# Kernel optimization log

Measured on AMD Instinct MI355X. Metric: run time of the kernel, lower is better.

The kernel has to match this reference:

```python
import jax, jax.numpy as jnp
import numpy as np
from functools import partial

D_MODEL = 1024
D_STATE = 16
D_CONV = 4
EXPAND = 2
DIM = EXPAND * D_MODEL  # 2048


def setup_inputs() -> dict:
    key = jax.random.key(0)
    ks = jax.random.split(key, 10)
    s = lambda fan_in: 1.0 / np.sqrt(fan_in)
    inp = {
        "x": jax.random.normal(ks[0], (8, 2048, D_MODEL), dtype=jnp.float32),
        "W_in": jax.random.normal(ks[1], (DIM, D_MODEL), dtype=jnp.float32) * s(D_MODEL),
        "b_in": jnp.zeros((DIM,), dtype=jnp.float32),
        "conv_w": jax.random.normal(ks[2], (DIM, 1, D_CONV), dtype=jnp.float32) * s(D_CONV),
        "conv_b": jnp.zeros((DIM,), dtype=jnp.float32),
        "W_x": jax.random.normal(ks[3], (3 * D_STATE, DIM), dtype=jnp.float32) * s(DIM),
        "W_dt": jax.random.normal(ks[4], (DIM, D_STATE), dtype=jnp.float32) * s(D_STATE),
        "b_dt": jnp.zeros((DIM,), dtype=jnp.float32),
        "W_out": jax.random.normal(ks[5], (D_MODEL, DIM), dtype=jnp.float32) * s(DIM),
        "b_out": jnp.zeros((D_MODEL,), dtype=jnp.float32),
    }
    return inp


def _selective_scan(xc, delta, A, Bm, Cm):
    # xc, delta: (B, L, DIM); Bm, Cm: (B, L, N); A: (N,)
    Bsz = xc.shape[0]
    h0 = jnp.zeros((Bsz, DIM, D_STATE), dtype=xc.dtype)

    def step(h, inputs):
        xc_t, d_t, b_t, c_t = inputs  # (B,DIM),(B,DIM),(B,N),(B,N)
        h = h * jnp.exp(d_t[:, :, None] * A) + xc_t[:, :, None] * b_t[:, None, :]
        y_t = jnp.einsum("bdn,bn->bd", h, c_t)
        return h, y_t

    tm = lambda a: jnp.swapaxes(a, 0, 1)  # time-major
    _, ys = jax.lax.scan(step, h0, (tm(xc), tm(delta), tm(Bm), tm(Cm)))
    return jnp.swapaxes(ys, 0, 1)  # (B, L, DIM)


def reference(x, W_in, b_in, conv_w, conv_b, W_x, W_dt, b_dt, W_out, b_out):
    A = -jnp.exp(jnp.linspace(0.0, -5.0, D_STATE).astype(x.dtype))  # (N,)
    xp = x @ W_in.T + b_in  # (B, L, DIM)
    # depthwise conv1d, padding=D_CONV-1 on BOTH sides (as torch Conv1d) -> length L+D_CONV-1
    xc = jax.lax.conv_general_dilated(
        jnp.swapaxes(xp, 1, 2), conv_w,
        window_strides=(1,), padding=[(D_CONV - 1, D_CONV - 1)],
        feature_group_count=DIM,
        dimension_numbers=("NCH", "OIH", "NCH"),
    ) + conv_b[None, :, None]
    xc = jnp.swapaxes(xc, 1, 2)  # (B, Lc, DIM)
    x_dbl = xc @ W_x.T  # (B, Lc, 3N)
    d_raw, Bm, Cm = jnp.split(x_dbl, [D_STATE, 2 * D_STATE], axis=-1)
    delta = jax.nn.softplus(d_raw @ W_dt.T + b_dt)  # (B, Lc, DIM)
    y = _selective_scan(xc, delta, A, Bm, Cm)  # (B, Lc, DIM)
    return y @ W_out.T + b_out  # (B, Lc, D_MODEL)
```

## Files before the change

### kernel.cpp

```cpp
#include <hip/hip_runtime.h>
#include <cstdint>
#include <cstddef>

#define B8 8
#define LSEQ 2048
#define LC 2051
#define DMODEL 1024
#define DIM 2048
#define LPAD 2054
#define M2 16408
#define M2P 16512
#define CS 32
#define NCH 65

typedef __attribute__((ext_vector_type(8))) short short8;
typedef __attribute__((ext_vector_type(4))) float floatx4;
typedef __attribute__((ext_vector_type(2))) float float2v;
typedef __attribute__((address_space(3))) unsigned short lds_ushort;

__device__ __constant__ float AeT[16] = {
  -1.0f,          -0.71653131f, -0.51341712f, -0.36787944f,
  -0.26359714f,   -0.18887560f, -0.13533528f, -0.09697208f,
  -0.06948345f,   -0.04978707f, -0.03567399f, -0.02556154f,
  -0.01831564f,   -0.01312373f, -0.00940356f, -0.00673795f};

#define LOG2E 1.44269504088896f

__device__ __forceinline__ float bf2f(unsigned short h) {
  union { unsigned int u; float f; } v; v.u = ((unsigned int)h) << 16; return v.f;
}
__device__ __forceinline__ unsigned short f2bf(float f) {
  union { float f; unsigned int u; } v; v.f = f;
  unsigned int r = (v.u + 0x7FFFu + ((v.u >> 16) & 1u)) >> 16;
  return (unsigned short)r;
}

__device__ __forceinline__ float2v pk_mul_vv(float2v a, float2v b) {
  float2v d; asm("v_pk_mul_f32 %0, %1, %2" : "=v"(d) : "v"(a), "v"(b)); return d;
}
__device__ __forceinline__ float2v pk_mul_sv(float2v bs, float2v a) {
  float2v d; asm("v_pk_mul_f32 %0, %1, %2" : "=v"(d) : "s"(bs), "v"(a)); return d;
}
__device__ __forceinline__ float2v pk_fma_vvv(float2v a, float2v b, float2v c) {
  float2v d; asm("v_pk_fma_f32 %0, %1, %2, %3" : "=v"(d) : "v"(a), "v"(b), "v"(c)); return d;
}
__device__ __forceinline__ float2v pk_fma_vsv(float2v a, float2v bs, float2v c) {
  float2v d; asm("v_pk_fma_f32 %0, %1, %2, %3" : "=v"(d) : "v"(a), "s"(bs), "v"(c)); return d;
}
__device__ __forceinline__ float2v pk_add_vv(float2v a, float2v b) {
  float2v d; asm("v_pk_add_f32 %0, %1, %2" : "=v"(d) : "v"(a), "v"(b)); return d;
}
__device__ __forceinline__ float exp2_raw(float x) {
  float d; asm("v_exp_f32 %0, %1" : "=v"(d) : "v"(x)); return d;
}

__device__ __forceinline__ short8 ds_read_b128_(const lds_ushort* p) {
  floatx4 d;
  unsigned addr = (unsigned)(size_t)p;
  asm volatile("ds_read_b128 %0, %1" : "=v"(d) : "v"(addr));
  return __builtin_bit_cast(short8, d);
}

__global__ __launch_bounds__(256) void init_kernel(const float* __restrict__ x,
                                                   const float* __restrict__ W_in,
                                                   const float* __restrict__ W_out,
                                                   const float* __restrict__ W_x,
                                                   unsigned short* __restrict__ xA,
                                                   unsigned short* __restrict__ wInB,
                                                   unsigned short* __restrict__ wOutB,
                                                   unsigned short* __restrict__ wXB,
                                                   unsigned short* __restrict__ xp) {
  const int gid = blockIdx.x;
  const float* in; unsigned short* out; int i;
  if (gid < 8192)        { in = x;     out = xA;    i = gid * 256 + threadIdx.x; }
  else if (gid < 9216)   { in = W_in;  out = wInB;  i = (gid - 8192) * 256 + threadIdx.x; }
  else if (gid < 10240)  { in = W_out; out = wOutB; i = (gid - 9216) * 256 + threadIdx.x; }
  else if (gid < 10288)  { in = W_x;   out = wXB;   i = (gid - 10240) * 256 + threadIdx.x; }
  else {
    int ii = (gid - 10288) * 256 + threadIdx.x;
    int b = ii / 1536;
    int r6 = (ii % 1536) / 256;
    int dd = (ii % 256) * 8;
    int row = (r6 < 3) ? r6 : (2048 + r6);
    *(uint4*)(xp + ((size_t)b * LPAD + row) * DIM + dd) = make_uint4(0, 0, 0, 0);
    return;
  }
  const float4* p = (const float4*)in + (size_t)i * 2;
  float4 a = p[0], b = p[1];
  uint4 o;
  o.x = (unsigned)f2bf(a.x) | ((unsigned)f2bf(a.y) << 16);
  o.y = (unsigned)f2bf(a.z) | ((unsigned)f2bf(a.w) << 16);
  o.z = (unsigned)f2bf(b.x) | ((unsigned)f2bf(b.y) << 16);
  o.w = (unsigned)f2bf(b.z) | ((unsigned)f2bf(b.w) << 16);
  *((uint4*)out + i) = o;
}

__global__ __launch_bounds__(256) void conv_kernel(const unsigned short* __restrict__ xp,
                                                   const float* __restrict__ conv_w,
                                                   const float* __restrict__ conv_b,
                                                   unsigned short* __restrict__ xc) {
  const int tc0 = blockIdx.x * 16;
  const int b = blockIdx.y;
  const int d0 = threadIdx.x * 8;

  float4 cw[8];
#pragma unroll
  for (int j = 0; j < 8; ++j) cw[j] = *(const float4*)(conv_w + (size_t)(d0 + j) * 4);
  float cb[8];
  {
    const float4* cb4 = (const float4*)(conv_b + d0);
    float4 c0 = cb4[0], c1 = cb4[1];
    cb[0] = c0.x; cb[1] = c0.y; cb[2] = c0.z; cb[3] = c0.w;
    cb[4] = c1.x; cb[5] = c1.y; cb[6] = c1.z; cb[7] = c1.w;
  }

  const unsigned short* base = xp + ((size_t)b * LPAD + tc0) * DIM + d0;
  unsigned short* outp = xc + ((size_t)b * LC + tc0) * DIM + d0;

  auto loadrow = [&](float (&w)[8], int r) {
    uint4 v = *(const uint4*)(base + (size_t)r * DIM);
    w[0] = bf2f(v.x & 0xffff); w[1] = bf2f(v.x >> 16);
    w[2] = bf2f(v.y & 0xffff); w[3] = bf2f(v.y >> 16);
    w[4] = bf2f(v.z & 0xffff); w[5] = bf2f(v.z >> 16);
    w[6] = bf2f(v.w & 0xffff); w[7] = bf2f(v.w >> 16);
  };

  float wa[8], wb[8], wc[8];
  loadrow(wa, 0); loadrow(wb, 1); loadrow(wc, 2);
#pragma unroll
  for (int i = 0; i < 16; ++i) {
    float wd[8];
    loadrow(wd, i + 3);
    if (tc0 + i < LC) {
      float acc[8];
#pragma unroll
      for (int j = 0; j < 8; ++j) {
        acc[j] = cb[j];
        acc[j] = fmaf(wa[j], cw[j].x, acc[j]);
        acc[j] = fmaf(wb[j], cw[j].y, acc[j]);
        acc[j] = fmaf(wc[j], cw[j].z, acc[j]);
        acc[j] = fmaf(wd[j], cw[j].w, acc[j]);
      }
      uint4 o;
      o.x = (unsigned)f2bf(acc[0]) | ((unsigned)f2bf(acc[1]) << 16);
      o.y = (unsigned)f2bf(acc[2]) | ((unsigned)f2bf(acc[3]) << 16);
      o.z = (unsigned)f2bf(acc[4]) | ((unsigned)f2bf(acc[5]) << 16);
      o.w = (unsigned)f2bf(acc[6]) | ((unsigned)f2bf(acc[7]) << 16);
      *(uint4*)(outp + (size_t)i * DIM) = o;
    }
#pragma unroll
    for (int j = 0; j < 8; ++j) { wa[j] = wb[j]; wb[j] = wc[j]; wc[j] = wd[j]; }
  }
}

#define GAS(p) ((const __attribute__((address_space(1))) void*)(p))
#define LAS(p) ((__attribute__((address_space(3))) void*)(p))

template <int MODE, int NBM, int NBN, int LX, int TAIL, int SPLITK>
__global__ __launch_bounds__(256) void gemm_bt(const unsigned short* __restrict__ A,
                                               const unsigned short* __restrict__ Bw,
                                               const float* __restrict__ bias,
                                               void* __restrict__ Cout, int K) {
  const int gid = blockIdx.x;
  const int mainBlocks = 8 * LX * NBN;
  int bm, bn, ks = 0;
  if constexpr (SPLITK) {
    ks = gid & 7;
    bm = gid >> 3;
    bn = 0;
  } else if (TAIL && gid >= mainBlocks) {
    const int e = gid - mainBlocks;
    bm = 8 * LX + e / NBN;
    bn = e % NBN;
  } else {
    const int xcd = gid & 7;
    const int j = gid >> 3;
    bm = xcd * LX + (j % LX);
    bn = j / LX;
  }
  if (bm >= NBM) return;

  __shared__ __align__(16) unsigned short As[2][128 * 64];
  __shared__ __align__(16) unsigned short Bs[2][128 * 64];
  const int tid = threadIdx.x;
  const int lane = tid & 63, wave = tid >> 6;
  const int wr = wave >> 1, wc = wave & 1;

  floatx4 acc[4][4];
#pragma unroll
  for (int i = 0; i < 4; ++i)
#pragma unroll
    for (int j2 = 0; j2 < 4; ++j2) acc[i][j2] = (floatx4){0.f, 0.f, 0.f, 0.f};

  const int srow = tid >> 3;
  const int scol = ((tid & 7) ^ ((tid >> 3) & 7)) * 8;
  const unsigned short* Ab[4];
  const unsigned short* Bb[4];
#pragma unroll
  for (int L = 0; L < 4; ++L) {
    Ab[L] = A  + (size_t)(bm * 128 + L * 32 + srow) * K + scol;
    Bb[L] = Bw + (size_t)(bn * 128 + L * 32 + srow) * K + scol;
  }

  const int fr = lane & 15;
  const int hi = lane >> 4;
  const int fx = fr & 7;

  auto STAGE = [&](int buf, int k0) {
#pragma unroll
    for (int L = 0; L < 4; ++L) {
      __builtin_amdgcn_global_load_lds(GAS(Ab[L] + k0), LAS(&As[buf][L * 2048 + tid * 8]), 16, 0, 0);
      __builtin_amdgcn_global_load_lds(GAS(Bb[L] + k0), LAS(&Bs[buf][L * 2048 + tid * 8]), 16, 0, 0);
    }
  };

  const int kbase = SPLITK ? ks * (K >> 3) : 0;
  const int NT = (SPLITK ? (K >> 3) : K) >> 6;
  STAGE(0, kbase);
  asm volatile("s_waitcnt vmcnt(0)");
  __syncthreads();

  int cur = 0;
  for (int t = 0; t < NT; ++t) {
    if (t + 1 < NT) STAGE(cur ^ 1, kbase + (t + 1) * 64);

    const lds_ushort* tA = (const lds_ushort*)LAS(&As[cur][0]);
    const lds_ushort* tB = (const lds_ushort*)LAS(&Bs[cur][0]);
#pragma unroll
    for (int kk = 0; kk < 2; ++kk) {
      const int pb = ((kk * 4 + hi) ^ fx) * 8;
      short8 af[4], bf[4];
#pragma unroll
      for (int mt = 0; mt < 4; ++mt) af[mt] = ds_read_b128_(tA + (wr * 64 + mt * 16 + fr) * 64 + pb);
#pragma unroll
      for (int nt = 0; nt < 4; ++nt) bf[nt] = ds_read_b128_(tB + (wc * 64 + nt * 16 + fr) * 64 + pb);
      asm volatile("s_waitcnt lgkmcnt(0)");
      __builtin_amdgcn_sched_barrier(0);
      __builtin_amdgcn_s_setprio(1);
#pragma unroll
      for (int mt = 0; mt < 4; ++mt)
#pragma unroll
        for (int nt = 0; nt < 4; ++nt)
          acc[mt][nt] = __builtin_amdgcn_mfma_f32_16x16x32_bf16(af[mt], bf[nt], acc[mt][nt], 0, 0, 0);
      __builtin_amdgcn_s_setprio(0);
    }
    __syncthreads();
    cur ^= 1;
  }

  const int er = (lane >> 4) * 4, ec = lane & 15;
#pragma unroll
  for (int mt = 0; mt < 4; ++mt) {
#pragma unroll
    for (int nt = 0; nt < 4; ++nt) {
#pragma unroll
      for (int i = 0; i < 4; ++i) {
        int r = bm * 128 + wr * 64 + mt * 16 + er + i;
        int c = bn * 128 + wc * 64 + nt * 16 + ec;
        float v = acc[mt][nt][i];
        if constexpr (MODE == 0) {
          int bb = r >> 11, t = r & 2047;
          ((unsigned short*)Cout)[((size_t)bb * LPAD + 3 + t) * DIM + c] = f2bf(v + bias[c]);
        } else if constexpr (MODE == 1) {
          if (c < 48) ((float*)Cout)[((size_t)ks * M2P + r) * 48 + c] = v;
        } else {
          if (r < M2) ((float*)Cout)[(size_t)r * DMODEL + c] = v + bias[c];
        }
      }
    }
  }
}

__global__ __launch_bounds__(256) void reduce_xdbl(const float* __restrict__ part,
                                                   float* __restrict__ xdbl) {
  int i = blockIdx.x * 256 + threadIdx.x;
  if (i >= 196896) return;
  float4 s = make_float4(0.f, 0.f, 0.f, 0.f);
#pragma unroll
  for (int ks = 0; ks < 8; ++ks) {
    float4 v = *(const float4*)(part + (size_t)ks * M2P * 48 + (size_t)i * 4);
    s.x += v.x; s.y += v.y; s.z += v.z; s.w += v.w;
  }
  *(float4*)(xdbl + (size_t)i * 4) = s;
}

__global__ __launch_bounds__(256) void delta_kernel(const float* __restrict__ xdbl,
                                                    const float* __restrict__ W_dt,
                                                    const float* __restrict__ b_dt,
                                                    unsigned short* __restrict__ delta) {
  const int d = blockIdx.y * 256 + threadIdx.x;
  const int r0 = blockIdx.x * 8;
  float wv[16];
  const float4* wp = (const float4*)(W_dt + (size_t)d * 16);
#pragma unroll
  for (int q = 0; q < 4; ++q) {
    float4 t = wp[q];
    wv[q * 4 + 0] = t.x; wv[q * 4 + 1] = t.y; wv[q * 4 + 2] = t.z; wv[q * 4 + 3] = t.w;
  }
  const float bd = b_dt[d];
#pragma unroll
  for (int j = 0; j < 8; ++j) {
    const float* dr = xdbl + (size_t)(r0 + j) * 48;
    float z0 = bd, z1 = 0.f, z2 = 0.f, z3 = 0.f;
#pragma unroll
    for (int n = 0; n < 16; n += 4) {
      z0 = fmaf(dr[n + 0], wv[n + 0], z0);
      z1 = fmaf(dr[n + 1], wv[n + 1], z1);
      z2 = fmaf(dr[n + 2], wv[n + 2], z2);
      z3 = fmaf(dr[n + 3], wv[n + 3], z3);
    }
    float z = (z0 + z1) + (z2 + z3);
    float dl = (z > 20.f) ? z : __logf(1.f + __expf(z));
    delta[(size_t)(r0 + j) * DIM + d] = f2bf(dl);
  }
}

__global__ __launch_bounds__(256) void scan_pass1(const unsigned short* __restrict__ xc,
                                                  const unsigned short* __restrict__ dl,
                                                  const float* __restrict__ xd,
                                                  unsigned short* __restrict__ sdbuf,
                                                  unsigned short* __restrict__ qbuf) {
  const int wid = __builtin_amdgcn_readfirstlane((int)(threadIdx.x >> 6));
  const int lane = threadIdx.x & 63;
  const int W = blockIdx.x * 4 + wid;
  const int dg = W & 31;
  const int rest = W >> 5;
  const int c = rest % NCH;
  const int b = rest / NCH;
  const int d = dg * 64 + lane;
  const int t0 = c * CS;
  const int nst = (t0 + CS <= LC) ? CS : (LC - t0);

  float2v A2L[8];
#pragma unroll
  for (int i = 0; i < 8; ++i)
    A2L[i] = (float2v){AeT[2 * i] * LOG2E, AeT[2 * i + 1] * LOG2E};

  float2v h2[8];
#pragma unroll
  for (int i = 0; i < 8; ++i) h2[i] = (float2v){0.f, 0.f};
  float sumd = 0.f;

  const size_t row0 = (size_t)b * LC + t0;
  const float* xdb = xd + row0 * 48 + 16;
  const unsigned short* xcp = xc + row0 * DIM + d;
  const unsigned short* dp  = dl + row0 * DIM + d;

  auto body = [&](int s) {
    float2v Bv[8];
#pragma unroll
    for (int j = 0; j < 8; ++j) Bv[j] = *(const float2v*)(xdb + (size_t)s * 48 + 2 * j);
    float dlt = bf2f(dp[(size_t)s * DIM]);
    float xcv = bf2f(xcp[(size_t)s * DIM]);
    sumd += dlt;
    float2v dlt2 = (float2v){dlt, dlt};
    float2v xcv2 = (float2v){xcv, xcv};
#pragma unroll
    for (int i = 0; i < 8; ++i) {
      float2v arg = pk_mul_vv(dlt2, A2L[i]);
      float e0 = exp2_raw(arg.x), e1 = exp2_raw(arg.y);
      float2v e2 = (float2v){e0, e1};
      h2[i] = pk_fma_vvv(h2[i], e2, pk_mul_sv(Bv[i], xcv2));
    }
  };

  if (nst == CS) {
#pragma unroll
    for (int s = 0; s < CS; ++s) body(s);
  } else {
    for (int s = 0; s < nst; ++s) body(s);
  }

  sdbuf[((size_t)(b * NCH + c) << 11) + d] = f2bf(sumd);
  const size_t base = ((size_t)(b * NCH + c) * 16) * 2048 + d;
#pragma unroll
  for (int i = 0; i < 8; ++i) {
    qbuf[base + ((size_t)(2 * i) << 11)]     = f2bf(h2[i].x);
    qbuf[base + ((size_t)(2 * i + 1) << 11)] = f2bf(h2[i].y);
  }
}

__global__ __launch_bounds__(256) void scan_boundary(const unsigned short* __restrict__ sdbuf,
                                                     unsigned short* __restrict__ qbuf) {
  const int tid = threadIdx.x;
  const int n = tid >> 4;
  const int d = blockIdx.x * 16 + (tid & 15);
  const int b = blockIdx.y;
  const float aL = AeT[n] * LOG2E;
  float h = 0.f;
  for (int c = 0; c < NCH; ++c) {
    const size_t sbase = ((size_t)(b * NCH + c) << 11);
    const float sd = bf2f(sdbuf[sbase + d]);
    const size_t base = (sbase << 4) + ((size_t)n << 11) + d;
    const float qv = bf2f(qbuf[base]);
    const float Pv = exp2_raw(sd * aL);
    qbuf[base] = f2bf(h);
    h = fmaf(Pv, h, qv);
  }
}

__global__ __launch_bounds__(256) void scan_pass2(const unsigned short* __restrict__ xc,
                                                  const unsigned short* __restrict__ dl,
                                                  const float* __restrict__ xd,
                                                  const unsigned short* __restrict__ hinit,
                                                  unsigned short* __restrict__ y) {
  const int wid = __builtin_amdgcn_readfirstlane((int)(threadIdx.x >> 6));
  const int lane = threadIdx.x & 63;
  const int W = blockIdx.x * 4 + wid;
  const int dg = W & 31;
  const int rest = W >> 5;
  const int c = rest % NCH;
  const int b = rest / NCH;
  const int d = dg * 64 + lane;
  const int t0 = c * CS;
  const int nst = (t0 + CS <= LC) ? CS : (LC - t0);

  float2v A2L[8];
#pragma unroll
  for (int i = 0; i < 8; ++i)
    A2L[i] = (float2v){AeT[2 * i] * LOG2E, AeT[2 * i + 1] * LOG2E};

  const size_t base = ((size_t)(b * NCH + c) * 16) * 2048 + d;
  float2v h2[8];
#pragma unroll
  for (int i = 0; i < 8; ++i)
    h2[i] = (float2v){bf2f(hinit[base + ((size_t)(2 * i) << 11)]),
                      bf2f(hinit[base + ((size_t)(2 * i + 1) << 11)])};

  const size_t row0 = (size_t)b * LC + t0;
  const float* xdb = xd + row0 * 48 + 16;
  const unsigned short* xcp = xc + row0 * DIM + d;
  const unsigned short* dp  = dl + row0 * DIM + d;
  unsigned short* yp = y + row0 * DIM + d;

  auto body = [&](int s) {
    float2v Bv[8], Cv[8];
#pragma unroll
    for (int j = 0; j < 8; ++j) {
      Bv[j] = *(const float2v*)(xdb + (size_t)s * 48 + 2 * j);
      Cv[j] = *(const float2v*)(xdb + (size_t)s * 48 + 16 + 2 * j);
    }
    float dlt = bf2f(dp[(size_t)s * DIM]);
    float xcv = bf2f(xcp[(size_t)s * DIM]);
    float2v dlt2 = (float2v){dlt, dlt};
    float2v xcv2 = (float2v){xcv, xcv};
    float2v y2[4];
#pragma unroll
    for (int i = 0; i < 4; ++i) y2[i] = (float2v){0.f, 0.f};
#pragma unroll
    for (int i = 0; i < 8; ++i) {
      float2v arg = pk_mul_vv(dlt2, A2L[i]);
      float e0 = exp2_raw(arg.x), e1 = exp2_raw(arg.y);
      float2v e2 = (float2v){e0, e1};
      h2[i] = pk_fma_vvv(h2[i], e2, pk_mul_sv(Bv[i], xcv2));
      y2[i & 3] = pk_fma_vsv(h2[i], Cv[i], y2[i & 3]);
    }
    float2v s01 = pk_add_vv(y2[0], y2[1]);
    float2v s23 = pk_add_vv(y2[2], y2[3]);
    float2v st = pk_add_vv(s01, s23);
    yp[(size_t)s * DIM] = f2bf(st.x + st.y);
  };

  if (nst == CS) {
#pragma unroll
    for (int s = 0; s < CS; ++s) body(s);
  } else {
    for (int s = 0; s < nst; ++s) body(s);
  }
}

extern "C" void kernel_launch(void* const* d_in, const int* in_sizes, int n_in,
                              void* d_out, int out_size, void* d_ws, size_t ws_size,
                              hipStream_t stream) {
  const float* x      = (const float*)d_in[0];
  const float* W_in   = (const float*)d_in[1];
  const float* b_in   = (const float*)d_in[2];
  const float* conv_w = (const float*)d_in[3];
  const float* conv_b = (const float*)d_in[4];
  const float* W_x    = (const float*)d_in[5];
  const float* W_dt   = (const float*)d_in[6];
  const float* b_dt   = (const float*)d_in[7];
  const float* W_out  = (const float*)d_in[8];
  const float* b_out  = (const float*)d_in[9];

  char* w = (char*)d_ws;
  unsigned short* xp    = (unsigned short*)w;
  unsigned short* delta = (unsigned short*)w;
  unsigned short* ybuf  = (unsigned short*)w;
  size_t off = (size_t)M2P * DIM * 2;
  unsigned short* xcb  = (unsigned short*)(w + off); off += (size_t)M2P * DIM * 2;
  size_t xA_off = off;
  unsigned short* xA   = (unsigned short*)(w + off); off += (size_t)16384 * 1024 * 2;
  unsigned short* wInB = (unsigned short*)(w + off); off += (size_t)2048 * 1024 * 2;
  unsigned short* wOutB= (unsigned short*)(w + off); off += (size_t)1024 * 2048 * 2;
  unsigned short* wXB  = (unsigned short*)(w + off); off += (size_t)128 * 2048 * 2;
  float* xdbl          = (float*)(w + off);          off += (size_t)M2 * 48 * 4;
  float* part           = (float*)(w + xA_off);
  unsigned short* sdbuf = (unsigned short*)(w + xA_off);
  unsigned short* qbuf  = (unsigned short*)(w + xA_off + (size_t)B8 * NCH * 2048 * 2);
  (void)ws_size; (void)in_sizes; (void)n_in; (void)out_size;

  init_kernel<<<10336, 256, 0, stream>>>(x, W_in, W_out, W_x, xA, wInB, wOutB, wXB, xp);

  gemm_bt<0, 128, 16, 16, 0, 0><<<2048, 256, 0, stream>>>(xA, wInB, b_in, xp, 1024);
  conv_kernel<<<dim3(129, B8), 256, 0, stream>>>(xp, conv_w, conv_b, xcb);
  gemm_bt<1, 129, 1, 0, 0, 1><<<1032, 256, 0, stream>>>(xcb, wXB, nullptr, part, 2048);
  reduce_xdbl<<<770, 256, 0, stream>>>(part, xdbl);
  delta_kernel<<<dim3(2051, 8), 256, 0, stream>>>(xdbl, W_dt, b_dt, delta);

  scan_pass1<<<4160, 256, 0, stream>>>(xcb, delta, xdbl, sdbuf, qbuf);
  scan_boundary<<<dim3(128, B8), 256, 0, stream>>>(sdbuf, qbuf);
  scan_pass2<<<4160, 256, 0, stream>>>(xcb, delta, xdbl, qbuf, ybuf);

  gemm_bt<2, 129, 8, 16, 1, 0><<<1032, 256, 0, stream>>>(ybuf, wOutB, b_out, (float*)d_out, 2048);
}
```

Baseline: 511.3 us.

## Fuse delta projection into scan passes and single-buffer GEMM LDS tiles

After: 566.6 us. +10.8%, slower.

```diff
diff --git a/kernel.cpp b/kernel.cpp
--- a/kernel.cpp
+++ b/kernel.cpp
@@ -16,7 +16,6 @@
 typedef __attribute__((ext_vector_type(8))) short short8;
 typedef __attribute__((ext_vector_type(4))) float floatx4;
 typedef __attribute__((ext_vector_type(2))) float float2v;
-typedef __attribute__((address_space(3))) unsigned short lds_ushort;
 
 __device__ __constant__ float AeT[16] = {
   -1.0f,          -0.71653131f, -0.51341712f, -0.36787944f,
@@ -52,13 +51,6 @@
 }
 __device__ __forceinline__ float exp2_raw(float x) {
   float d; asm("v_exp_f32 %0, %1" : "=v"(d) : "v"(x)); return d;
-}
-
-__device__ __forceinline__ short8 ds_read_b128_(const lds_ushort* p) {
-  floatx4 d;
-  unsigned addr = (unsigned)(size_t)p;
-  asm volatile("ds_read_b128 %0, %1" : "=v"(d) : "v"(addr));
-  return __builtin_bit_cast(short8, d);
 }
 
 __global__ __launch_bounds__(256) void init_kernel(const float* __restrict__ x,
@@ -180,8 +172,8 @@
   }
   if (bm >= NBM) return;
 
-  __shared__ __align__(16) unsigned short As[2][128 * 64];
-  __shared__ __align__(16) unsigned short Bs[2][128 * 64];
+  __shared__ __align__(16) unsigned short As[128 * 64];
+  __shared__ __align__(16) unsigned short Bs[128 * 64];
   const int tid = threadIdx.x;
   const int lane = tid & 63, wave = tid >> 6;
   const int wr = wave >> 1, wc = wave & 1;
@@ -206,46 +198,32 @@
   const int hi = lane >> 4;
   const int fx = fr & 7;
 
-  auto STAGE = [&](int buf, int k0) {
+  const int kbase = SPLITK ? ks * (K >> 3) : 0;
+  const int kend = kbase + (SPLITK ? (K >> 3) : K);
+
+  for (int k0 = kbase; k0 < kend; k0 += 64) {
+    __syncthreads();
 #pragma unroll
     for (int L = 0; L < 4; ++L) {
-      __builtin_amdgcn_global_load_lds(GAS(Ab[L] + k0), LAS(&As[buf][L * 2048 + tid * 8]), 16, 0, 0);
-      __builtin_amdgcn_global_load_lds(GAS(Bb[L] + k0), LAS(&Bs[buf][L * 2048 + tid * 8]), 16, 0, 0);
-    }
-  };
-
-  const int kbase = SPLITK ? ks * (K >> 3) : 0;
-  const int NT = (SPLITK ? (K >> 3) : K) >> 6;
-  STAGE(0, kbase);
-  asm volatile("s_waitcnt vmcnt(0)");
-  __syncthreads();
-
-  int cur = 0;
-  for (int t = 0; t < NT; ++t) {
-    if (t + 1 < NT) STAGE(cur ^ 1, kbase + (t + 1) * 64);
-
-    const lds_ushort* tA = (const lds_ushort*)LAS(&As[cur][0]);
-    const lds_ushort* tB = (const lds_ushort*)LAS(&Bs[cur][0]);
+      __builtin_amdgcn_global_load_lds(GAS(Ab[L] + k0), LAS(As + L * 2048 + tid * 8), 16, 0, 0);
+      __builtin_amdgcn_global_load_lds(GAS(Bb[L] + k0), LAS(Bs + L * 2048 + tid * 8), 16, 0, 0);
+    }
+    __syncthreads();
+
 #pragma unroll
     for (int kk = 0; kk < 2; ++kk) {
       const int pb = ((kk * 4 + hi) ^ fx) * 8;
       short8 af[4], bf[4];
 #pragma unroll
-      for (int mt = 0; mt < 4; ++mt) af[mt] = ds_read_b128_(tA + (wr * 64 + mt * 16 + fr) * 64 + pb);
-#pragma unroll
-      for (int nt = 0; nt < 4; ++nt) bf[nt] = ds_read_b128_(tB + (wc * 64 + nt * 16 + fr) * 64 + pb);
-      asm volatile("s_waitcnt lgkmcnt(0)");
-      __builtin_amdgcn_sched_barrier(0);
-      __builtin_amdgcn_s_setprio(1);
+      for (int mt = 0; mt < 4; ++mt) af[mt] = *(const short8*)&As[(wr * 64 + mt * 16 + fr) * 64 + pb];
+#pragma unroll
+      for (int nt = 0; nt < 4; ++nt) bf[nt] = *(const short8*)&Bs[(wc * 64 + nt * 16 + fr) * 64 + pb];
 #pragma unroll
       for (int mt = 0; mt < 4; ++mt)
 #pragma unroll
         for (int nt = 0; nt < 4; ++nt)
           acc[mt][nt] = __builtin_amdgcn_mfma_f32_16x16x32_bf16(af[mt], bf[nt], acc[mt][nt], 0, 0, 0);
-      __builtin_amdgcn_s_setprio(0);
-    }
-    __syncthreads();
-    cur ^= 1;
+    }
   }
 
   const int er = (lane >> 4) * 4, ec = lane & 15;
@@ -284,40 +262,10 @@
   *(float4*)(xdbl + (size_t)i * 4) = s;
 }
 
-__global__ __launch_bounds__(256) void delta_kernel(const float* __restrict__ xdbl,
-                                                    const float* __restrict__ W_dt,
-                                                    const float* __restrict__ b_dt,
-                                                    unsigned short* __restrict__ delta) {
-  const int d = blockIdx.y * 256 + threadIdx.x;
-  const int r0 = blockIdx.x * 8;
-  float wv[16];
-  const float4* wp = (const float4*)(W_dt + (size_t)d * 16);
-#pragma unroll
-  for (int q = 0; q < 4; ++q) {
-    float4 t = wp[q];
-    wv[q * 4 + 0] = t.x; wv[q * 4 + 1] = t.y; wv[q * 4 + 2] = t.z; wv[q * 4 + 3] = t.w;
-  }
-  const float bd = b_dt[d];
-#pragma unroll
-  for (int j = 0; j < 8; ++j) {
-    const float* dr = xdbl + (size_t)(r0 + j) * 48;
-    float z0 = bd, z1 = 0.f, z2 = 0.f, z3 = 0.f;
-#pragma unroll
-    for (int n = 0; n < 16; n += 4) {
-      z0 = fmaf(dr[n + 0], wv[n + 0], z0);
-      z1 = fmaf(dr[n + 1], wv[n + 1], z1);
-      z2 = fmaf(dr[n + 2], wv[n + 2], z2);
-      z3 = fmaf(dr[n + 3], wv[n + 3], z3);
-    }
-    float z = (z0 + z1) + (z2 + z3);
-    float dl = (z > 20.f) ? z : __logf(1.f + __expf(z));
-    delta[(size_t)(r0 + j) * DIM + d] = f2bf(dl);
-  }
-}
-
 __global__ __launch_bounds__(256) void scan_pass1(const unsigned short* __restrict__ xc,
-                                                  const unsigned short* __restrict__ dl,
                                                   const float* __restrict__ xd,
+                                                  const float* __restrict__ W_dt,
+                                                  const float* __restrict__ b_dt,
                                                   unsigned short* __restrict__ sdbuf,
                                                   unsigned short* __restrict__ qbuf) {
   const int wid = __builtin_amdgcn_readfirstlane((int)(threadIdx.x >> 6));
@@ -336,21 +284,38 @@
   for (int i = 0; i < 8; ++i)
     A2L[i] = (float2v){AeT[2 * i] * LOG2E, AeT[2 * i + 1] * LOG2E};
 
+  float2v wdt2[8];
+  {
+    const float4* wp = (const float4*)(W_dt + (size_t)d * 16);
+#pragma unroll
+    for (int q = 0; q < 4; ++q) {
+      float4 t = wp[q];
+      wdt2[q * 2 + 0] = (float2v){t.x, t.y};
+      wdt2[q * 2 + 1] = (float2v){t.z, t.w};
+    }
+  }
+  const float bd = b_dt[d];
+
   float2v h2[8];
 #pragma unroll
   for (int i = 0; i < 8; ++i) h2[i] = (float2v){0.f, 0.f};
   float sumd = 0.f;
 
   const size_t row0 = (size_t)b * LC + t0;
-  const float* xdb = xd + row0 * 48 + 16;
+  const float* xdb = xd + row0 * 48;
   const unsigned short* xcp = xc + row0 * DIM + d;
-  const unsigned short* dp  = dl + row0 * DIM + d;
 
   auto body = [&](int s) {
-    float2v Bv[8];
-#pragma unroll
-    for (int j = 0; j < 8; ++j) Bv[j] = *(const float2v*)(xdb + (size_t)s * 48 + 2 * j);
-    float dlt = bf2f(dp[(size_t)s * DIM]);
+    const float* xr = xdb + (size_t)s * 48;
+    float2v z2[4];
+#pragma unroll
+    for (int i = 0; i < 4; ++i) z2[i] = (float2v){0.f, 0.f};
+#pragma unroll
+    for (int i = 0; i < 8; ++i)
+      z2[i & 3] = pk_fma_vsv(wdt2[i], *(const float2v*)(xr + 2 * i), z2[i & 3]);
+    float2v zt = pk_add_vv(pk_add_vv(z2[0], z2[1]), pk_add_vv(z2[2], z2[3]));
+    float z = bd + zt.x + zt.y;
+    float dlt = (z > 20.f) ? z : __logf(1.f + __expf(z));
     float xcv = bf2f(xcp[(size_t)s * DIM]);
     sumd += dlt;
     float2v dlt2 = (float2v){dlt, dlt};
@@ -360,7 +325,7 @@
       float2v arg = pk_mul_vv(dlt2, A2L[i]);
       float e0 = exp2_raw(arg.x), e1 = exp2_raw(arg.y);
       float2v e2 = (float2v){e0, e1};
-      h2[i] = pk_fma_vvv(h2[i], e2, pk_mul_sv(Bv[i], xcv2));
+      h2[i] = pk_fma_vvv(h2[i], e2, pk_mul_sv(*(const float2v*)(xr + 16 + 2 * i), xcv2));
     }
   };
 
@@ -400,8 +365,9 @@
 }
 
 __global__ __launch_bounds__(256) void scan_pass2(const unsigned short* __restrict__ xc,
-                                                  const unsigned short* __restrict__ dl,
                                                   const float* __restrict__ xd,
+                                                  const float* __restrict__ W_dt,
+                                                  const float* __restrict__ b_dt,
                                                   const unsigned short* __restrict__ hinit,
                                                   unsigned short* __restrict__ y) {
   const int wid = __builtin_amdgcn_readfirstlane((int)(threadIdx.x >> 6));
@@ -420,6 +386,18 @@
   for (int i = 0; i < 8; ++i)
     A2L[i] = (float2v){AeT[2 * i] * LOG2E, AeT[2 * i + 1] * LOG2E};
 
+  float2v wdt2[8];
+  {
+    const float4* wp = (const float4*)(W_dt + (size_t)d * 16);
+#pragma unroll
+    for (int q = 0; q < 4; ++q) {
+      float4 t = wp[q];
+      wdt2[q * 2 + 0] = (float2v){t.x, t.y};
+      wdt2[q * 2 + 1] = (float2v){t.z, t.w};
+    }
+  }
+  const float bd = b_dt[d];
+
   const size_t base = ((size_t)(b * NCH + c) * 16) * 2048 + d;
   float2v h2[8];
 #pragma unroll
@@ -428,19 +406,21 @@
                       bf2f(hinit[base + ((size_t)(2 * i + 1) << 11)])};
 
   const size_t row0 = (size_t)b * LC + t0;
-  const float* xdb = xd + row0 * 48 + 16;
+  const float* xdb = xd + row0 * 48;
   const unsigned short* xcp = xc + row0 * DIM + d;
-  const unsigned short* dp  = dl + row0 * DIM + d;
   unsigned short* yp = y + row0 * DIM + d;
 
   auto body = [&](int s) {
-    float2v Bv[8], Cv[8];
-#pragma unroll
-    for (int j = 0; j < 8; ++j) {
-      Bv[j] = *(const float2v*)(xdb + (size_t)s * 48 + 2 * j);
-      Cv[j] = *(const float2v*)(xdb + (size_t)s * 48 + 16 + 2 * j);
-    }
-    float dlt = bf2f(dp[(size_t)s * DIM]);
+    const float* xr = xdb + (size_t)s * 48;
+    float2v z2[4];
+#pragma unroll
+    for (int i = 0; i < 4; ++i) z2[i] = (float2v){0.f, 0.f};
+#pragma unroll
+    for (int i = 0; i < 8; ++i)
+      z2[i & 3] = pk_fma_vsv(wdt2[i], *(const float2v*)(xr + 2 * i), z2[i & 3]);
+    float2v zt = pk_add_vv(pk_add_vv(z2[0], z2[1]), pk_add_vv(z2[2], z2[3]));
+    float z = bd + zt.x + zt.y;
+    float dlt = (z > 20.f) ? z : __logf(1.f + __expf(z));
     float xcv = bf2f(xcp[(size_t)s * DIM]);
     float2v dlt2 = (float2v){dlt, dlt};
     float2v xcv2 = (float2v){xcv, xcv};
@@ -452,8 +432,8 @@
       float2v arg = pk_mul_vv(dlt2, A2L[i]);
       float e0 = exp2_raw(arg.x), e1 = exp2_raw(arg.y);
       float2v e2 = (float2v){e0, e1};
-      h2[i] = pk_fma_vvv(h2[i], e2, pk_mul_sv(Bv[i], xcv2));
-      y2[i & 3] = pk_fma_vsv(h2[i], Cv[i], y2[i & 3]);
+      h2[i] = pk_fma_vvv(h2[i], e2, pk_mul_sv(*(const float2v*)(xr + 16 + 2 * i), xcv2));
+      y2[i & 3] = pk_fma_vsv(h2[i], *(const float2v*)(xr + 32 + 2 * i), y2[i & 3]);
     }
     float2v s01 = pk_add_vv(y2[0], y2[1]);
     float2v s23 = pk_add_vv(y2[2], y2[3]);
@@ -485,7 +465,6 @@
 
   char* w = (char*)d_ws;
   unsigned short* xp    = (unsigned short*)w;
-  unsigned short* delta = (unsigned short*)w;
   unsigned short* ybuf  = (unsigned short*)w;
   size_t off = (size_t)M2P * DIM * 2;
   unsigned short* xcb  = (unsigned short*)(w + off); off += (size_t)M2P * DIM * 2;
@@ -506,11 +485,10 @@
   conv_kernel<<<dim3(129, B8), 256, 0, stream>>>(xp, conv_w, conv_b, xcb);
   gemm_bt<1, 129, 1, 0, 0, 1><<<1032, 256, 0, stream>>>(xcb, wXB, nullptr, part, 2048);
   reduce_xdbl<<<770, 256, 0, stream>>>(part, xdbl);
-  delta_kernel<<<dim3(2051, 8), 256, 0, stream>>>(xdbl, W_dt, b_dt, delta);
-
-  scan_pass1<<<4160, 256, 0, stream>>>(xcb, delta, xdbl, sdbuf, qbuf);
+
+  scan_pass1<<<4160, 256, 0, stream>>>(xcb, xdbl, W_dt, b_dt, sdbuf, qbuf);
   scan_boundary<<<dim3(128, B8), 256, 0, stream>>>(sdbuf, qbuf);
-  scan_pass2<<<4160, 256, 0, stream>>>(xcb, delta, xdbl, qbuf, ybuf);
+  scan_pass2<<<4160, 256, 0, stream>>>(xcb, xdbl, W_dt, b_dt, qbuf, ybuf);
 
   gemm_bt<2, 129, 8, 16, 1, 0><<<1032, 256, 0, stream>>>(ybuf, wOutB, b_out, (float*)d_out, 2048);
 }
```
